# Kernel optimization log

Hardware: AMD Instinct MI355X
Metric: run time of the kernel (lower is better)

The kernel has to match this reference:

```python
import jax, jax.numpy as jnp
import numpy as np

EMBED_DIM = 768
NUM_HEAD = 12
HEAD_DIM = EMBED_DIM // NUM_HEAD


def setup_inputs() -> dict:
    key = jax.random.key(0)
    ks = jax.random.split(key, 9)
    B, S, E = 1, 4096, EMBED_DIM
    s = 1.0 / np.sqrt(E)
    inp = {
        "x": jax.random.normal(ks[0], (B, S, E), dtype=jnp.float32),
        "mask": jnp.zeros((B, S), dtype=jnp.bool_),  # True = masked out (padding)
        "Wq": jax.random.normal(ks[1], (E, E), dtype=jnp.float32) * s,
        "bq": jnp.zeros((E,), dtype=jnp.float32),
        "Wk": jax.random.normal(ks[2], (E, E), dtype=jnp.float32) * s,
        "bk": jnp.zeros((E,), dtype=jnp.float32),
        "Wv": jax.random.normal(ks[3], (E, E), dtype=jnp.float32) * s,
        "bv": jnp.zeros((E,), dtype=jnp.float32),
        "Wo": jax.random.normal(ks[4], (E, E), dtype=jnp.float32) * s,
        "bo": jnp.zeros((E,), dtype=jnp.float32),
    }
    return inp


def reference(x, mask, Wq, bq, Wk, bk, Wv, bv, Wo, bo):
    B, S, E = x.shape
    H, D = NUM_HEAD, HEAD_DIM
    # QKV projections -> [B, H, S, D]
    q = (x @ Wq.T + bq).reshape(B, S, H, D).transpose(0, 2, 1, 3)
    k = (x @ Wk.T + bk).reshape(B, S, H, D).transpose(0, 2, 1, 3)
    v = (x @ Wv.T + bv).reshape(B, S, H, D).transpose(0, 2, 1, 3)
    # NOTE: original scales by sqrt(embed_dim), not sqrt(head_dim)
    attn = jnp.einsum("bhqd,bhkd->bhqk", q, k) / jnp.sqrt(jnp.float32(E))
    # mask: [B, S] -> broadcast over (head, query) dims; True -> -inf
    attn = jnp.where(mask[:, None, None, :], -jnp.inf, attn)
    attn = jax.nn.softmax(attn, axis=-1)  # same math as manual max-subtract softmax
    out = jnp.einsum("bhqk,bhkd->bhqd", attn, v)  # [B, H, S, D]
    out = out.transpose(0, 2, 1, 3).reshape(B, S, E)
    return out @ Wo.T + bo
```

## Files before the change

kernel.cpp:

```cpp
#include <hip/hip_runtime.h>
#include <hip/hip_bf16.h>
#include <math.h>

typedef __bf16 bf16;
typedef __attribute__((ext_vector_type(8))) __bf16 bf16x8;
typedef __attribute__((ext_vector_type(4))) __bf16 bf16x4;
typedef __attribute__((ext_vector_type(4))) float f32x4;
typedef __attribute__((ext_vector_type(16))) float f32x16;

typedef __attribute__((address_space(1))) void* as1ptr;
typedef __attribute__((address_space(3))) void* as3ptr;

__device__ __forceinline__ void gload16(const void* g, void* lds) {
  __builtin_amdgcn_global_load_lds((as1ptr)(unsigned long long)(g),
                                   (as3ptr)(unsigned long long)(lds), 16, 0, 0);
}

#define MFMA16(a, b, c) __builtin_amdgcn_mfma_f32_16x16x32_bf16((a), (b), (c), 0, 0, 0)
#define MFMA32(a, b, c) __builtin_amdgcn_mfma_f32_32x32x16_bf16((a), (b), (c), 0, 0, 0)
#define EXP2(x) __builtin_amdgcn_exp2f(x)
#define WAITV4 asm volatile("s_waitcnt vmcnt(4)" ::: "memory")
#define WAITV2 asm volatile("s_waitcnt vmcnt(2)" ::: "memory")
#define WAITV0 asm volatile("s_waitcnt vmcnt(0)" ::: "memory")
#define BAR() __builtin_amdgcn_s_barrier()
#define PRIO1() __builtin_amdgcn_s_setprio(1)
#define PRIO0() __builtin_amdgcn_s_setprio(0)

#define SEQ 4096
#define EMB 768
#define QSC (0.036084391824351615f * 1.4426950408889634f)

#define NCVT 2688
__global__ __launch_bounds__(256)
void cvt_all_kernel(const float* __restrict__ x, const float* __restrict__ Wq,
                    const float* __restrict__ Wk, const float* __restrict__ Wv,
                    const float* __restrict__ Wo,
                    bf16* __restrict__ xb, bf16* __restrict__ Wqb, bf16* __restrict__ Wkb,
                    bf16* __restrict__ Wvb, bf16* __restrict__ Wob,
                    const unsigned char* __restrict__ mask,
                    unsigned long long* __restrict__ tf64) {
  int b = blockIdx.x;
  if (b == NCVT) {
    int t = threadIdx.x;
    if (t < 64) {
      unsigned v = 0;
      const unsigned char* mp = mask + t * 64;
      for (int i = 0; i < 64; i++) v |= mp[i];
      unsigned long long bits = __ballot(v != 0);
      if (t == 0) *tf64 = bits;
    }
    return;
  }
  const float* in;
  bf16* out;
  int base;
  if (b < 1536) {
    in = x; out = xb; base = b;
  } else {
    int r = b - 1536, seg = r / 288, off = r % 288;
    in  = (seg == 0) ? Wq  : (seg == 1) ? Wk  : (seg == 2) ? Wv  : Wo;
    out = (seg == 0) ? Wqb : (seg == 1) ? Wkb : (seg == 2) ? Wvb : Wob;
    base = off;
  }
  int i = (base * 256 + threadIdx.x) * 8;
  float4 a = *(const float4*)(in + i);
  float4 c = *(const float4*)(in + i + 4);
  bf16x8 v;
  v[0] = (bf16)a.x; v[1] = (bf16)a.y; v[2] = (bf16)a.z; v[3] = (bf16)a.w;
  v[4] = (bf16)c.x; v[5] = (bf16)c.y; v[6] = (bf16)c.z; v[7] = (bf16)c.w;
  *(bf16x8*)(out + i) = v;
}

template <int MODE>
__global__ __launch_bounds__(256)
void gemm_bt_kernel(const bf16* __restrict__ A,
                    const bf16* __restrict__ B0, const bf16* __restrict__ B1,
                    const bf16* __restrict__ B2,
                    const float* __restrict__ bias0, const float* __restrict__ bias1,
                    const float* __restrict__ bias2,
                    float* __restrict__ outF, bf16* __restrict__ Qh,
                    char* __restrict__ Kswz, char* __restrict__ Vswz) {
  __shared__ __attribute__((aligned(16))) char Asb[3][8192];
  __shared__ __attribute__((aligned(16))) char Bsb[3][8192];
  const int tid = threadIdx.x;
  const int wid = tid >> 6, lane = tid & 63;
  const int g = lane >> 4, c16 = lane & 15;
  const int wr = wid >> 1, wc = wid & 1;
  const int bm0 = blockIdx.x * 128;

  const bf16* Bp;
  const float* bias;
  int nb, mat = 0;
  if (MODE == 1) {
    mat = blockIdx.y / 6;
    nb = (blockIdx.y % 6) * 128;
    Bp = (mat == 0) ? B0 : (mat == 1 ? B1 : B2);
    bias = (mat == 0) ? bias0 : (mat == 1 ? bias1 : bias2);
  } else {
    nb = blockIdx.y * 128;
    Bp = B0;
    bias = bias0;
  }

  const int arow = tid >> 2, acol = (tid & 3) * 16;

#define STAGE_G(k, b)                                                              \
  do {                                                                             \
    gload16((const char*)A + (size_t)(bm0 + arow) * (EMB * 2) + (k)*64 + acol,     \
            &Asb[b][wid * 1024]);                                                  \
    gload16((const char*)A + (size_t)(bm0 + 64 + arow) * (EMB * 2) + (k)*64 + acol,\
            &Asb[b][4096 + wid * 1024]);                                           \
    gload16((const char*)Bp + (size_t)(nb + arow) * (EMB * 2) + (k)*64 + acol,     \
            &Bsb[b][wid * 1024]);                                                  \
    gload16((const char*)Bp + (size_t)(nb + 64 + arow) * (EMB * 2) + (k)*64 + acol,\
            &Bsb[b][4096 + wid * 1024]);                                           \
  } while (0)

  f32x4 acc[4][4];
#pragma unroll
  for (int i = 0; i < 4; i++)
#pragma unroll
    for (int j = 0; j < 4; j++) acc[i][j] = f32x4{0.f, 0.f, 0.f, 0.f};

#define COMPUTE_G(cur)                                                         \
  do {                                                                         \
    bf16x8 a[4], b[4];                                                         \
    _Pragma("unroll") for (int i = 0; i < 4; i++)                              \
        a[i] = *(const bf16x8*)(&Asb[cur][(wr * 64 + i * 16 + c16) * 64 + g * 16]); \
    _Pragma("unroll") for (int j = 0; j < 4; j++)                              \
        b[j] = *(const bf16x8*)(&Bsb[cur][(wc * 64 + j * 16 + c16) * 64 + g * 16]); \
    PRIO1();                                                                   \
    _Pragma("unroll") for (int i = 0; i < 4; i++)                              \
        _Pragma("unroll") for (int j = 0; j < 4; j++)                          \
            acc[i][j] = MFMA16(a[i], b[j], acc[i][j]);                         \
    PRIO0();                                                                   \
  } while (0)

  STAGE_G(0, 0);
  STAGE_G(1, 1);
  int cur = 0;
  for (int kk = 0; kk < EMB / 32 - 1; ++kk) {
    WAITV4;
    BAR();
    if (kk < EMB / 32 - 2) {
      int stb = (cur == 0) ? 2 : cur - 1;
      STAGE_G(kk + 2, stb);
    }
    COMPUTE_G(cur);
    cur = (cur == 2) ? 0 : cur + 1;
  }
  WAITV0;
  BAR();
  COMPUTE_G(cur);
#undef STAGE_G
#undef COMPUTE_G

#pragma unroll
  for (int i = 0; i < 4; i++) {
#pragma unroll
    for (int j = 0; j < 4; j++) {
      int colL = nb + wc * 64 + j * 16 + c16;
      float bval = bias[colL];
#pragma unroll
      for (int r = 0; r < 4; r++) {
        int row = bm0 + wr * 64 + i * 16 + 4 * g + r;
        float val = acc[i][j][r] + bval;
        if (MODE == 0) {
          outF[(size_t)row * EMB + colL] = val;
        } else {
          int hh = colL >> 6, d = colL & 63;
          if (mat == 0) {
            Qh[((size_t)hh * SEQ + row) * 64 + d] = (bf16)(val * QSC);
          } else if (mat == 1) {
            *(bf16*)(Kswz + ((size_t)hh * SEQ + row) * 128 +
                     ((d * 2) ^ ((row & 7) << 4))) = (bf16)val;
          } else {
            int kk2 = row & 63;
            int cc = (kk2 & 48) | (kk2 & 3) | ((kk2 & 4) << 1) | ((kk2 & 8) >> 1);
            *(bf16*)(Vswz + ((size_t)hh * 64 + d) * 8192 + (size_t)(row >> 6) * 128 +
                     ((cc * 2) ^ ((d & 7) << 4))) = (bf16)val;
          }
        }
      }
    }
  }
}

__global__ __launch_bounds__(512)
void attn_kernel(const char* __restrict__ Kswz, const char* __restrict__ Vswz,
                 const bf16* __restrict__ Qh, const unsigned char* __restrict__ mask,
                 const unsigned long long* __restrict__ tf64,
                 bf16* __restrict__ P0, bf16* __restrict__ P1, float* __restrict__ lm) {
  __shared__ __attribute__((aligned(16))) char LBUF[49152];
  char* LK = LBUF;
  char* LV = LBUF + 24576;
  const int tid = threadIdx.x;
  const int wid = tid >> 6, lane = tid & 63;
  const int qh = wid >> 1, kh = wid & 1;
  const int l31 = lane & 31, hi = lane >> 5;
  const int bsw = ((blockIdx.x & 7) * 96) + (blockIdx.x >> 3);
  const int h = bsw >> 6;
  const int rem = bsw & 63;
  const int qb = rem >> 1;
  const int ks = rem & 1;
  const unsigned long long tfb = *tf64;
  const int NT = 32;

  bf16x8 qa[4];
  {
    const bf16* qp = Qh + ((size_t)h * SEQ + qb * 128 + qh * 32 + l31) * 64 + hi * 8;
    qa[0] = *(const bf16x8*)(qp);
    qa[1] = *(const bf16x8*)(qp + 16);
    qa[2] = *(const bf16x8*)(qp + 32);
    qa[3] = *(const bf16x8*)(qp + 48);
  }

  f32x16 ot0, ot1;
#pragma unroll
  for (int r = 0; r < 16; r++) { ot0[r] = 0.f; ot1[r] = 0.f; }
  float m_ = -1e38f, l_ = 0.f;

  const char* ksrc = Kswz + (size_t)h * SEQ * 128 + (size_t)ks * 2048 * 128 + tid * 16;
  const char* vsrc = Vswz + ((size_t)h * 64 + (tid >> 3)) * 8192 + ks * 4096 + (tid & 7) * 16;

#define STAGE(t, b)                                              \
  do {                                                           \
    gload16(ksrc + (size_t)(t)*8192, LK + (b)*8192 + wid * 1024);\
    gload16(vsrc + (size_t)(t)*128,  LV + (b)*8192 + wid * 1024);\
  } while (0)

  const int krow = kh * 32 + l31;
  const int ksw = (krow & 7) << 4;
  const int vsw = (l31 & 7) << 4;
  const int vcb = kh * 64 + hi * 16;

#define COMPUTE(t, cur)                                                          \
  do {                                                                           \
    const char* Kb = LK + (cur)*8192;                                            \
    const char* Vb = LV + (cur)*8192;                                            \
    bf16x8 kf0 = *(const bf16x8*)(Kb + krow * 128 + ((hi * 16) ^ ksw));          \
    bf16x8 kf1 = *(const bf16x8*)(Kb + krow * 128 + ((32 + hi * 16) ^ ksw));     \
    bf16x8 kf2 = *(const bf16x8*)(Kb + krow * 128 + ((64 + hi * 16) ^ ksw));     \
    bf16x8 kf3 = *(const bf16x8*)(Kb + krow * 128 + ((96 + hi * 16) ^ ksw));     \
    f32x16 s;                                                                    \
    _Pragma("unroll") for (int r = 0; r < 16; r++) s[r] = 0.f;                   \
    PRIO1();                                                                     \
    s = MFMA32(kf0, qa[0], s);                                                   \
    s = MFMA32(kf1, qa[1], s);                                                   \
    s = MFMA32(kf2, qa[2], s);                                                   \
    s = MFMA32(kf3, qa[3], s);                                                   \
    PRIO0();                                                                     \
    if (tfb & (1ull << (ks * 32 + (t)))) {                                       \
      _Pragma("unroll") for (int r = 0; r < 16; r++) {                           \
        int key = ks * 2048 + (t)*64 + kh * 32 + (r & 3) + 8 * (r >> 2) + 4 * hi;\
        if (mask[key]) s[r] = -INFINITY;                                         \
      }                                                                          \
    }                                                                            \
    float m01 = fmaxf(fmaxf(s[0], s[1]), fmaxf(s[2], s[3]));                     \
    float m23 = fmaxf(fmaxf(s[4], s[5]), fmaxf(s[6], s[7]));                     \
    float m45 = fmaxf(fmaxf(s[8], s[9]), fmaxf(s[10], s[11]));                   \
    float m67 = fmaxf(fmaxf(s[12], s[13]), fmaxf(s[14], s[15]));                 \
    float mt = fmaxf(fmaxf(m01, m23), fmaxf(m45, m67));                          \
    mt = fmaxf(mt, __shfl_xor(mt, 32));                                          \
    if (__any(mt > m_ + 8.f)) {                                                  \
      float mn = fmaxf(m_, mt);                                                  \
      float corr = EXP2(m_ - mn);                                                \
      l_ *= corr;                                                                \
      ot0 *= corr;                                                               \
      ot1 *= corr;                                                               \
      m_ = mn;                                                                   \
    }                                                                            \
    float p[16];                                                                 \
    _Pragma("unroll") for (int r = 0; r < 16; r++) p[r] = EXP2(s[r] - m_);       \
    float ls = (((p[0] + p[1]) + (p[2] + p[3])) + ((p[4] + p[5]) + (p[6] + p[7]))) + \
               (((p[8] + p[9]) + (p[10] + p[11])) + ((p[12] + p[13]) + (p[14] + p[15]))); \
    ls += __shfl_xor(ls, 32);                                                    \
    l_ += ls;                                                                    \
    bf16x8 pb0, pb1;                                                             \
    _Pragma("unroll") for (int e = 0; e < 8; ++e) {                              \
      pb0[e] = (bf16)p[e];                                                       \
      pb1[e] = (bf16)p[8 + e];                                                   \
    }                                                                            \
    bf16x8 vf00 = *(const bf16x8*)(Vb + l31 * 128 + ((vcb) ^ vsw));              \
    bf16x8 vf01 = *(const bf16x8*)(Vb + l31 * 128 + ((vcb + 32) ^ vsw));         \
    bf16x8 vf10 = *(const bf16x8*)(Vb + (32 + l31) * 128 + ((vcb) ^ vsw));       \
    bf16x8 vf11 = *(const bf16x8*)(Vb + (32 + l31) * 128 + ((vcb + 32) ^ vsw));  \
    PRIO1();                                                                     \
    ot0 = MFMA32(vf00, pb0, ot0);                                                \
    ot0 = MFMA32(vf01, pb1, ot0);                                                \
    ot1 = MFMA32(vf10, pb0, ot1);                                                \
    ot1 = MFMA32(vf11, pb1, ot1);                                                \
    PRIO0();                                                                     \
  } while (0)

  STAGE(0, 0);
  STAGE(1, 1);
  int cur = 0;
  for (int t = 0; t < NT - 1; ++t) {
    WAITV2;
    BAR();
    if (t < NT - 2) {
      int stb = (cur == 0) ? 2 : cur - 1;
      STAGE(t + 2, stb);
    }
    COMPUTE(t, cur);
    cur = (cur == 2) ? 0 : cur + 1;
  }
  WAITV0;
  BAR();
  COMPUTE(NT - 1, cur);
#undef STAGE
#undef COMPUTE

  __syncthreads();
  float* ml = (float*)(LBUF + 32768);
  ml[(wid * 64 + lane) * 2 + 0] = m_;
  ml[(wid * 64 + lane) * 2 + 1] = l_;
  __syncthreads();
  const int pw = wid ^ 1;
  float m2 = ml[(pw * 64 + lane) * 2 + 0];
  float l2 = ml[(pw * 64 + lane) * 2 + 1];
  float M = fmaxf(m_, m2);
  float al = EXP2(m_ - M);
  float lt = al * l_ + EXP2(m2 - M) * l2;
  ot0 *= al;
  ot1 *= al;
  char* obase = LBUF + qh * 8192 + lane * 128;
  const int osw = (lane & 7) << 4;
  if (kh == 1) {
#pragma unroll
    for (int u = 0; u < 4; ++u) {
      f32x4 w0 = {ot0[4 * u], ot0[4 * u + 1], ot0[4 * u + 2], ot0[4 * u + 3]};
      f32x4 w1 = {ot1[4 * u], ot1[4 * u + 1], ot1[4 * u + 2], ot1[4 * u + 3]};
      *(f32x4*)(obase + ((u * 16) ^ osw)) = w0;
      *(f32x4*)(obase + (((4 + u) * 16) ^ osw)) = w1;
    }
  }
  __syncthreads();
  if (kh == 0) {
    float inv = 1.f / lt;
    int tok = qb * 128 + qh * 32 + l31;
    bf16* Op = ks ? P1 : P0;
    bf16* op = Op + (size_t)tok * EMB + h * 64;
#pragma unroll
    for (int u = 0; u < 4; ++u) {
      f32x4 w0 = *(const f32x4*)(obase + ((u * 16) ^ osw));
      f32x4 w1 = *(const f32x4*)(obase + (((4 + u) * 16) ^ osw));
      bf16x4 o0, o1;
#pragma unroll
      for (int e = 0; e < 4; ++e) {
        o0[e] = (bf16)((ot0[4 * u + e] + w0[e]) * inv);
        o1[e] = (bf16)((ot1[4 * u + e] + w1[e]) * inv);
      }
      *(bf16x4*)(op + 8 * u + 4 * hi) = o0;
      *(bf16x4*)(op + 32 + 8 * u + 4 * hi) = o1;
    }
    if (lane < 32) {
      float* lmp = lm + (((size_t)ks * 12 + h) * 4096 + tok) * 2;
      lmp[0] = M;
      lmp[1] = lt;
    }
  }
}

__global__ __launch_bounds__(256)
void merge_kernel(bf16* __restrict__ P0, const bf16* __restrict__ P1,
                  const float* __restrict__ lm) {
  int idx = (blockIdx.x * 256 + threadIdx.x) * 8;
  int tok = idx / EMB;
  int e0 = idx % EMB;
  int h = e0 >> 6;
  const float* l0p = lm + ((size_t)h * 4096 + tok) * 2;
  const float* l1p = lm + (((size_t)12 + h) * 4096 + tok) * 2;
  float m0 = l0p[0], l0 = l0p[1];
  float m1 = l1p[0], l1 = l1p[1];
  float M = fmaxf(m0, m1);
  float w0 = EXP2(m0 - M) * l0;
  float w1 = EXP2(m1 - M) * l1;
  float inv = 1.f / (w0 + w1);
  w0 *= inv;
  w1 *= inv;
  bf16x8 a = *(const bf16x8*)(P0 + idx);
  bf16x8 b = *(const bf16x8*)(P1 + idx);
  bf16x8 o;
#pragma unroll
  for (int e = 0; e < 8; ++e) o[e] = (bf16)(w0 * (float)a[e] + w1 * (float)b[e]);
  *(bf16x8*)(P0 + idx) = o;
}

extern "C" void kernel_launch(void* const* d_in, const int* in_sizes, int n_in,
                              void* d_out, int out_size, void* d_ws, size_t ws_size,
                              hipStream_t stream) {
  (void)in_sizes; (void)n_in; (void)out_size; (void)ws_size;
  const float* x = (const float*)d_in[0];
  const unsigned char* mask = (const unsigned char*)d_in[1];
  const float* Wq = (const float*)d_in[2];
  const float* bq = (const float*)d_in[3];
  const float* Wk = (const float*)d_in[4];
  const float* bk = (const float*)d_in[5];
  const float* Wv = (const float*)d_in[6];
  const float* bv = (const float*)d_in[7];
  const float* Wo = (const float*)d_in[8];
  const float* bo = (const float*)d_in[9];
  float* out = (float*)d_out;
  char* ws = (char*)d_ws;

  bf16* xb   = (bf16*)(ws + 0);
  bf16* Wqb  = (bf16*)(ws + 6291456);
  bf16* Wkb  = (bf16*)(ws + 7471104);
  bf16* Wvb  = (bf16*)(ws + 8650752);
  bf16* Wob  = (bf16*)(ws + 9830400);
  bf16* Qh   = (bf16*)(ws + 11010048);
  char* Kswz = ws + 17301504;
  char* Vswz = ws + 23592960;
  bf16* Obuf = (bf16*)(ws + 29884416);
  unsigned long long* tf64 = (unsigned long long*)(ws + 36175872);
  float* lmArr = (float*)(ws + 36179968);
  bf16* P1 = xb;

  cvt_all_kernel<<<NCVT + 1, 256, 0, stream>>>(x, Wq, Wk, Wv, Wo, xb, Wqb, Wkb, Wvb,
                                               Wob, mask, tf64);
  gemm_bt_kernel<1><<<dim3(32, 18), 256, 0, stream>>>(
      xb, Wqb, Wkb, Wvb, bq, bk, bv, nullptr, Qh, Kswz, Vswz);
  attn_kernel<<<768, 512, 0, stream>>>(Kswz, Vswz, Qh, mask, tf64, Obuf, P1, lmArr);
  merge_kernel<<<1536, 256, 0, stream>>>(Obuf, P1, lmArr);
  gemm_bt_kernel<0><<<dim3(32, 6), 256, 0, stream>>>(
      Obuf, Wob, nullptr, nullptr, bo, nullptr, nullptr, out, nullptr, nullptr, nullptr);
}
```

Measured before the change: 134.2 us.

## Process two query tiles per wave in attention and rotate K/V LDS layout

The attention kernel now runs 256 threads (4 waves) per block instead of 512. Each wave handles two 32-row query tiles, so every K and V fragment loaded from LDS feeds two MFMAs, and the staging loads per thread double. The K/V swizzle written by the projection GEMM gains a per-row block rotation, with matching read offsets, to spread LDS bank accesses. This raises register pressure from four output accumulators, and fewer waves per block may reduce latency hiding, which the launch bounds of 3 blocks per unit are meant to offset.

Measured after the change: 139.1 us. +3.7%, slower.

```diff
diff --git a/kernel.cpp b/kernel.cpp
--- a/kernel.cpp
+++ b/kernel.cpp
@@ -20,7 +20,6 @@
 #define MFMA32(a, b, c) __builtin_amdgcn_mfma_f32_32x32x16_bf16((a), (b), (c), 0, 0, 0)
 #define EXP2(x) __builtin_amdgcn_exp2f(x)
 #define WAITV4 asm volatile("s_waitcnt vmcnt(4)" ::: "memory")
-#define WAITV2 asm volatile("s_waitcnt vmcnt(2)" ::: "memory")
 #define WAITV0 asm volatile("s_waitcnt vmcnt(0)" ::: "memory")
 #define BAR() __builtin_amdgcn_s_barrier()
 #define PRIO1() __builtin_amdgcn_s_setprio(1)
@@ -172,13 +171,17 @@
           if (mat == 0) {
             Qh[((size_t)hh * SEQ + row) * 64 + d] = (bf16)(val * QSC);
           } else if (mat == 1) {
+            int blk = (((d * 2) >> 5) + (row >> 3)) & 3;
+            int off = blk * 32 + ((d * 2) & 31);
             *(bf16*)(Kswz + ((size_t)hh * SEQ + row) * 128 +
-                     ((d * 2) ^ ((row & 7) << 4))) = (bf16)val;
+                     (off ^ ((row & 7) << 4))) = (bf16)val;
           } else {
             int kk2 = row & 63;
             int cc = (kk2 & 48) | (kk2 & 3) | ((kk2 & 4) << 1) | ((kk2 & 8) >> 1);
+            int blk = (((cc * 2) >> 5) + (d >> 3)) & 3;
+            int off = blk * 32 + ((cc * 2) & 31);
             *(bf16*)(Vswz + ((size_t)hh * 64 + d) * 8192 + (size_t)(row >> 6) * 128 +
-                     ((cc * 2) ^ ((d & 7) << 4))) = (bf16)val;
+                     (off ^ ((d & 7) << 4))) = (bf16)val;
           }
         }
       }
@@ -186,7 +189,7 @@
   }
 }
 
-__global__ __launch_bounds__(512)
+__global__ __launch_bounds__(256, 3)
 void attn_kernel(const char* __restrict__ Kswz, const char* __restrict__ Vswz,
                  const bf16* __restrict__ Qh, const unsigned char* __restrict__ mask,
                  const unsigned long long* __restrict__ tf64,
@@ -206,90 +209,138 @@
   const unsigned long long tfb = *tf64;
   const int NT = 32;
 
-  bf16x8 qa[4];
+  bf16x8 qaA[4], qaB[4];
   {
-    const bf16* qp = Qh + ((size_t)h * SEQ + qb * 128 + qh * 32 + l31) * 64 + hi * 8;
-    qa[0] = *(const bf16x8*)(qp);
-    qa[1] = *(const bf16x8*)(qp + 16);
-    qa[2] = *(const bf16x8*)(qp + 32);
-    qa[3] = *(const bf16x8*)(qp + 48);
-  }
-
-  f32x16 ot0, ot1;
-#pragma unroll
-  for (int r = 0; r < 16; r++) { ot0[r] = 0.f; ot1[r] = 0.f; }
-  float m_ = -1e38f, l_ = 0.f;
+    const bf16* qp = Qh + ((size_t)h * SEQ + qb * 128 + qh * 64 + l31) * 64 + hi * 8;
+#pragma unroll
+    for (int j = 0; j < 4; ++j) {
+      qaA[j] = *(const bf16x8*)(qp + j * 16);
+      qaB[j] = *(const bf16x8*)(qp + 32 * 64 + j * 16);
+    }
+  }
+
+  f32x16 otA0, otA1, otB0, otB1;
+#pragma unroll
+  for (int r = 0; r < 16; r++) { otA0[r] = 0.f; otA1[r] = 0.f; otB0[r] = 0.f; otB1[r] = 0.f; }
+  float mA_ = -1e38f, lA_ = 0.f, mB_ = -1e38f, lB_ = 0.f;
 
   const char* ksrc = Kswz + (size_t)h * SEQ * 128 + (size_t)ks * 2048 * 128 + tid * 16;
   const char* vsrc = Vswz + ((size_t)h * 64 + (tid >> 3)) * 8192 + ks * 4096 + (tid & 7) * 16;
 
-#define STAGE(t, b)                                              \
-  do {                                                           \
-    gload16(ksrc + (size_t)(t)*8192, LK + (b)*8192 + wid * 1024);\
-    gload16(vsrc + (size_t)(t)*128,  LV + (b)*8192 + wid * 1024);\
+#define STAGE(t, b)                                                          \
+  do {                                                                       \
+    gload16(ksrc + (size_t)(t)*8192,        LK + (b)*8192 + wid * 1024);     \
+    gload16(ksrc + (size_t)(t)*8192 + 4096, LK + (b)*8192 + 4096 + wid * 1024); \
+    gload16(vsrc + (size_t)(t)*128,             LV + (b)*8192 + wid * 1024); \
+    gload16(vsrc + 32 * 8192 + (size_t)(t)*128, LV + (b)*8192 + 4096 + wid * 1024); \
   } while (0)
 
   const int krow = kh * 32 + l31;
   const int ksw = (krow & 7) << 4;
+  const int krot = (krow >> 3) & 3;
+  int kb_[4];
+#pragma unroll
+  for (int j = 0; j < 4; ++j) kb_[j] = ((((j + krot) & 3) * 32 + hi * 16) ^ ksw);
   const int vsw = (l31 & 7) << 4;
-  const int vcb = kh * 64 + hi * 16;
+  const int vrot = (l31 >> 3) & 3;
+  const int vb0 = (((kh * 2 + vrot) & 3) * 32 + hi * 16) ^ vsw;
+  const int vb1 = (((kh * 2 + 1 + vrot) & 3) * 32 + hi * 16) ^ vsw;
 
 #define COMPUTE(t, cur)                                                          \
   do {                                                                           \
     const char* Kb = LK + (cur)*8192;                                            \
     const char* Vb = LV + (cur)*8192;                                            \
-    bf16x8 kf0 = *(const bf16x8*)(Kb + krow * 128 + ((hi * 16) ^ ksw));          \
-    bf16x8 kf1 = *(const bf16x8*)(Kb + krow * 128 + ((32 + hi * 16) ^ ksw));     \
-    bf16x8 kf2 = *(const bf16x8*)(Kb + krow * 128 + ((64 + hi * 16) ^ ksw));     \
-    bf16x8 kf3 = *(const bf16x8*)(Kb + krow * 128 + ((96 + hi * 16) ^ ksw));     \
-    f32x16 s;                                                                    \
-    _Pragma("unroll") for (int r = 0; r < 16; r++) s[r] = 0.f;                   \
+    bf16x8 kf0 = *(const bf16x8*)(Kb + krow * 128 + kb_[0]);                     \
+    bf16x8 kf1 = *(const bf16x8*)(Kb + krow * 128 + kb_[1]);                     \
+    bf16x8 kf2 = *(const bf16x8*)(Kb + krow * 128 + kb_[2]);                     \
+    bf16x8 kf3 = *(const bf16x8*)(Kb + krow * 128 + kb_[3]);                     \
+    f32x16 sA, sB;                                                               \
+    _Pragma("unroll") for (int r = 0; r < 16; r++) { sA[r] = 0.f; sB[r] = 0.f; } \
     PRIO1();                                                                     \
-    s = MFMA32(kf0, qa[0], s);                                                   \
-    s = MFMA32(kf1, qa[1], s);                                                   \
-    s = MFMA32(kf2, qa[2], s);                                                   \
-    s = MFMA32(kf3, qa[3], s);                                                   \
+    sA = MFMA32(kf0, qaA[0], sA);                                                \
+    sB = MFMA32(kf0, qaB[0], sB);                                                \
+    sA = MFMA32(kf1, qaA[1], sA);                                                \
+    sB = MFMA32(kf1, qaB[1], sB);                                                \
+    sA = MFMA32(kf2, qaA[2], sA);                                                \
+    sB = MFMA32(kf2, qaB[2], sB);                                                \
+    sA = MFMA32(kf3, qaA[3], sA);                                                \
+    sB = MFMA32(kf3, qaB[3], sB);                                                \
     PRIO0();                                                                     \
     if (tfb & (1ull << (ks * 32 + (t)))) {                                       \
       _Pragma("unroll") for (int r = 0; r < 16; r++) {                           \
         int key = ks * 2048 + (t)*64 + kh * 32 + (r & 3) + 8 * (r >> 2) + 4 * hi;\
-        if (mask[key]) s[r] = -INFINITY;                                         \
+        if (mask[key]) { sA[r] = -INFINITY; sB[r] = -INFINITY; }                 \
       }                                                                          \
     }                                                                            \
-    float m01 = fmaxf(fmaxf(s[0], s[1]), fmaxf(s[2], s[3]));                     \
-    float m23 = fmaxf(fmaxf(s[4], s[5]), fmaxf(s[6], s[7]));                     \
-    float m45 = fmaxf(fmaxf(s[8], s[9]), fmaxf(s[10], s[11]));                   \
-    float m67 = fmaxf(fmaxf(s[12], s[13]), fmaxf(s[14], s[15]));                 \
-    float mt = fmaxf(fmaxf(m01, m23), fmaxf(m45, m67));                          \
-    mt = fmaxf(mt, __shfl_xor(mt, 32));                                          \
-    if (__any(mt > m_ + 8.f)) {                                                  \
-      float mn = fmaxf(m_, mt);                                                  \
-      float corr = EXP2(m_ - mn);                                                \
-      l_ *= corr;                                                                \
-      ot0 *= corr;                                                               \
-      ot1 *= corr;                                                               \
-      m_ = mn;                                                                   \
+    float mtA, mtB;                                                              \
+    {                                                                            \
+      float a0 = fmaxf(fmaxf(sA[0], sA[1]), fmaxf(sA[2], sA[3]));                \
+      float a1 = fmaxf(fmaxf(sA[4], sA[5]), fmaxf(sA[6], sA[7]));                \
+      float a2 = fmaxf(fmaxf(sA[8], sA[9]), fmaxf(sA[10], sA[11]));              \
+      float a3 = fmaxf(fmaxf(sA[12], sA[13]), fmaxf(sA[14], sA[15]));            \
+      mtA = fmaxf(fmaxf(a0, a1), fmaxf(a2, a3));                                 \
+      float b0 = fmaxf(fmaxf(sB[0], sB[1]), fmaxf(sB[2], sB[3]));                \
+      float b1 = fmaxf(fmaxf(sB[4], sB[5]), fmaxf(sB[6], sB[7]));                \
+      float b2 = fmaxf(fmaxf(sB[8], sB[9]), fmaxf(sB[10], sB[11]));              \
+      float b3 = fmaxf(fmaxf(sB[12], sB[13]), fmaxf(sB[14], sB[15]));            \
+      mtB = fmaxf(fmaxf(b0, b1), fmaxf(b2, b3));                                 \
     }                                                                            \
-    float p[16];                                                                 \
-    _Pragma("unroll") for (int r = 0; r < 16; r++) p[r] = EXP2(s[r] - m_);       \
-    float ls = (((p[0] + p[1]) + (p[2] + p[3])) + ((p[4] + p[5]) + (p[6] + p[7]))) + \
-               (((p[8] + p[9]) + (p[10] + p[11])) + ((p[12] + p[13]) + (p[14] + p[15]))); \
-    ls += __shfl_xor(ls, 32);                                                    \
-    l_ += ls;                                                                    \
-    bf16x8 pb0, pb1;                                                             \
-    _Pragma("unroll") for (int e = 0; e < 8; ++e) {                              \
-      pb0[e] = (bf16)p[e];                                                       \
-      pb1[e] = (bf16)p[8 + e];                                                   \
+    mtA = fmaxf(mtA, __shfl_xor(mtA, 32));                                       \
+    mtB = fmaxf(mtB, __shfl_xor(mtB, 32));                                       \
+    if (__any(mtA > mA_ + 8.f)) {                                                \
+      float mn = fmaxf(mA_, mtA);                                                \
+      float corr = EXP2(mA_ - mn);                                               \
+      lA_ *= corr;                                                               \
+      otA0 *= corr;                                                              \
+      otA1 *= corr;                                                              \
+      mA_ = mn;                                                                  \
     }                                                                            \
-    bf16x8 vf00 = *(const bf16x8*)(Vb + l31 * 128 + ((vcb) ^ vsw));              \
-    bf16x8 vf01 = *(const bf16x8*)(Vb + l31 * 128 + ((vcb + 32) ^ vsw));         \
-    bf16x8 vf10 = *(const bf16x8*)(Vb + (32 + l31) * 128 + ((vcb) ^ vsw));       \
-    bf16x8 vf11 = *(const bf16x8*)(Vb + (32 + l31) * 128 + ((vcb + 32) ^ vsw));  \
+    if (__any(mtB > mB_ + 8.f)) {                                                \
+      float mn = fmaxf(mB_, mtB);                                                \
+      float corr = EXP2(mB_ - mn);                                               \
+      lB_ *= corr;                                                               \
+      otB0 *= corr;                                                              \
+      otB1 *= corr;                                                              \
+      mB_ = mn;                                                                  \
+    }                                                                            \
+    bf16x8 pbA0, pbA1, pbB0, pbB1;                                               \
+    {                                                                            \
+      float p[16];                                                               \
+      _Pragma("unroll") for (int r = 0; r < 16; r++) p[r] = EXP2(sA[r] - mA_);   \
+      float ls = (((p[0] + p[1]) + (p[2] + p[3])) + ((p[4] + p[5]) + (p[6] + p[7]))) + \
+                 (((p[8] + p[9]) + (p[10] + p[11])) + ((p[12] + p[13]) + (p[14] + p[15]))); \
+      ls += __shfl_xor(ls, 32);                                                  \
+      lA_ += ls;                                                                 \
+      _Pragma("unroll") for (int e = 0; e < 8; ++e) {                            \
+        pbA0[e] = (bf16)p[e];                                                    \
+        pbA1[e] = (bf16)p[8 + e];                                                \
+      }                                                                          \
+    }                                                                            \
+    {                                                                            \
+      float p[16];                                                               \
+      _Pragma("unroll") for (int r = 0; r < 16; r++) p[r] = EXP2(sB[r] - mB_);   \
+      float ls = (((p[0] + p[1]) + (p[2] + p[3])) + ((p[4] + p[5]) + (p[6] + p[7]))) + \
+                 (((p[8] + p[9]) + (p[10] + p[11])) + ((p[12] + p[13]) + (p[14] + p[15]))); \
+      ls += __shfl_xor(ls, 32);                                                  \
+      lB_ += ls;                                                                 \
+      _Pragma("unroll") for (int e = 0; e < 8; ++e) {                            \
+        pbB0[e] = (bf16)p[e];                                                    \
+        pbB1[e] = (bf16)p[8 + e];                                                \
+      }                                                                          \
+    }                                                                            \
+    bf16x8 vf00 = *(const bf16x8*)(Vb + l31 * 128 + vb0);                        \
+    bf16x8 vf01 = *(const bf16x8*)(Vb + l31 * 128 + vb1);                        \
+    bf16x8 vf10 = *(const bf16x8*)(Vb + (32 + l31) * 128 + vb0);                 \
+    bf16x8 vf11 = *(const bf16x8*)(Vb + (32 + l31) * 128 + vb1);                 \
     PRIO1();                                                                     \
-    ot0 = MFMA32(vf00, pb0, ot0);                                                \
-    ot0 = MFMA32(vf01, pb1, ot0);                                                \
-    ot1 = MFMA32(vf10, pb0, ot1);                                                \
-    ot1 = MFMA32(vf11, pb1, ot1);                                                \
+    otA0 = MFMA32(vf00, pbA0, otA0);                                             \
+    otB0 = MFMA32(vf00, pbB0, otB0);                                             \
+    otA0 = MFMA32(vf01, pbA1, otA0);                                             \
+    otB0 = MFMA32(vf01, pbB1, otB0);                                             \
+    otA1 = MFMA32(vf10, pbA0, otA1);                                             \
+    otB1 = MFMA32(vf10, pbB0, otB1);                                             \
+    otA1 = MFMA32(vf11, pbA1, otA1);                                             \
+    otB1 = MFMA32(vf11, pbB1, otB1);                                             \
     PRIO0();                                                                     \
   } while (0)
 
@@ -297,7 +348,7 @@
   STAGE(1, 1);
   int cur = 0;
   for (int t = 0; t < NT - 1; ++t) {
-    WAITV2;
+    WAITV4;
     BAR();
     if (t < NT - 2) {
       int stb = (cur == 0) ? 2 : cur - 1;
@@ -314,51 +365,75 @@
 
   __syncthreads();
   float* ml = (float*)(LBUF + 32768);
-  ml[(wid * 64 + lane) * 2 + 0] = m_;
-  ml[(wid * 64 + lane) * 2 + 1] = l_;
+  {
+    float* p = ml + ((wid * 64 + lane) * 2) * 2;
+    p[0] = mA_; p[1] = lA_; p[2] = mB_; p[3] = lB_;
+  }
   __syncthreads();
   const int pw = wid ^ 1;
-  float m2 = ml[(pw * 64 + lane) * 2 + 0];
-  float l2 = ml[(pw * 64 + lane) * 2 + 1];
-  float M = fmaxf(m_, m2);
-  float al = EXP2(m_ - M);
-  float lt = al * l_ + EXP2(m2 - M) * l2;
-  ot0 *= al;
-  ot1 *= al;
-  char* obase = LBUF + qh * 8192 + lane * 128;
+  float ltA, ltB;
+  {
+    const float* p = ml + ((pw * 64 + lane) * 2) * 2;
+    float m2 = p[0], l2 = p[1];
+    float M = fmaxf(mA_, m2);
+    float al = EXP2(mA_ - M);
+    ltA = al * lA_ + EXP2(m2 - M) * l2;
+    otA0 *= al; otA1 *= al;
+    mA_ = M;
+    m2 = p[2]; l2 = p[3];
+    M = fmaxf(mB_, m2);
+    al = EXP2(mB_ - M);
+    ltB = al * lB_ + EXP2(m2 - M) * l2;
+    otB0 *= al; otB1 *= al;
+    mB_ = M;
+  }
+  char* baseA = LBUF + qh * 16384 + lane * 128;
+  char* baseB = LBUF + qh * 16384 + 8192 + lane * 128;
   const int osw = (lane & 7) << 4;
   if (kh == 1) {
 #pragma unroll
     for (int u = 0; u < 4; ++u) {
-      f32x4 w0 = {ot0[4 * u], ot0[4 * u + 1], ot0[4 * u + 2], ot0[4 * u + 3]};
-      f32x4 w1 = {ot1[4 * u], ot1[4 * u + 1], ot1[4 * u + 2], ot1[4 * u + 3]};
-      *(f32x4*)(obase + ((u * 16) ^ osw)) = w0;
-      *(f32x4*)(obase + (((4 + u) * 16) ^ osw)) = w1;
+      *(f32x4*)(baseA + ((u * 16) ^ osw)) =
+          f32x4{otA0[4 * u], otA0[4 * u + 1], otA0[4 * u + 2], otA0[4 * u + 3]};
+      *(f32x4*)(baseA + (((4 + u) * 16) ^ osw)) =
+          f32x4{otA1[4 * u], otA1[4 * u + 1], otA1[4 * u + 2], otA1[4 * u + 3]};
+      *(f32x4*)(baseB + ((u * 16) ^ osw)) =
+          f32x4{otB0[4 * u], otB0[4 * u + 1], otB0[4 * u + 2], otB0[4 * u + 3]};
+      *(f32x4*)(baseB + (((4 + u) * 16) ^ osw)) =
+          f32x4{otB1[4 * u], otB1[4 * u + 1], otB1[4 * u + 2], otB1[4 * u + 3]};
     }
   }
   __syncthreads();
   if (kh == 0) {
-    float inv = 1.f / lt;
-    int tok = qb * 128 + qh * 32 + l31;
     bf16* Op = ks ? P1 : P0;
-    bf16* op = Op + (size_t)tok * EMB + h * 64;
+    int tokA = qb * 128 + qh * 64 + l31;
+    float invA = 1.f / ltA, invB = 1.f / ltB;
+    bf16* opA = Op + (size_t)tokA * EMB + h * 64;
+    bf16* opB = Op + (size_t)(tokA + 32) * EMB + h * 64;
 #pragma unroll
     for (int u = 0; u < 4; ++u) {
-      f32x4 w0 = *(const f32x4*)(obase + ((u * 16) ^ osw));
-      f32x4 w1 = *(const f32x4*)(obase + (((4 + u) * 16) ^ osw));
-      bf16x4 o0, o1;
+      f32x4 wA0 = *(const f32x4*)(baseA + ((u * 16) ^ osw));
+      f32x4 wA1 = *(const f32x4*)(baseA + (((4 + u) * 16) ^ osw));
+      f32x4 wB0 = *(const f32x4*)(baseB + ((u * 16) ^ osw));
+      f32x4 wB1 = *(const f32x4*)(baseB + (((4 + u) * 16) ^ osw));
+      bf16x4 oA0, oA1, oB0, oB1;
 #pragma unroll
       for (int e = 0; e < 4; ++e) {
-        o0[e] = (bf16)((ot0[4 * u + e] + w0[e]) * inv);
-        o1[e] = (bf16)((ot1[4 * u + e] + w1[e]) * inv);
+        oA0[e] = (bf16)((otA0[4 * u + e] + wA0[e]) * invA);
+        oA1[e] = (bf16)((otA1[4 * u + e] + wA1[e]) * invA);
+        oB0[e] = (bf16)((otB0[4 * u + e] + wB0[e]) * invB);
+        oB1[e] = (bf16)((otB1[4 * u + e] + wB1[e]) * invB);
       }
-      *(bf16x4*)(op + 8 * u + 4 * hi) = o0;
-      *(bf16x4*)(op + 32 + 8 * u + 4 * hi) = o1;
+      *(bf16x4*)(opA + 8 * u + 4 * hi) = oA0;
+      *(bf16x4*)(opA + 32 + 8 * u + 4 * hi) = oA1;
+      *(bf16x4*)(opB + 8 * u + 4 * hi) = oB0;
+      *(bf16x4*)(opB + 32 + 8 * u + 4 * hi) = oB1;
     }
     if (lane < 32) {
-      float* lmp = lm + (((size_t)ks * 12 + h) * 4096 + tok) * 2;
-      lmp[0] = M;
-      lmp[1] = lt;
+      float* lmpA = lm + (((size_t)ks * 12 + h) * 4096 + tokA) * 2;
+      lmpA[0] = mA_; lmpA[1] = ltA;
+      float* lmpB = lm + (((size_t)ks * 12 + h) * 4096 + tokA + 32) * 2;
+      lmpB[0] = mB_; lmpB[1] = ltB;
     }
   }
 }
@@ -422,7 +497,7 @@
                                                Wob, mask, tf64);
   gemm_bt_kernel<1><<<dim3(32, 18), 256, 0, stream>>>(
       xb, Wqb, Wkb, Wvb, bq, bk, bv, nullptr, Qh, Kswz, Vswz);
-  attn_kernel<<<768, 512, 0, stream>>>(Kswz, Vswz, Qh, mask, tf64, Obuf, P1, lmArr);
+  attn_kernel<<<768, 256, 0, stream>>>(Kswz, Vswz, Qh, mask, tf64, Obuf, P1, lmArr);
   merge_kernel<<<1536, 256, 0, stream>>>(Obuf, P1, lmArr);
   gemm_bt_kernel<0><<<dim3(32, 6), 256, 0, stream>>>(
       Obuf, Wob, nullptr, nullptr, bo, nullptr, nullptr, out, nullptr, nullptr, nullptr);
```

## Software-pipeline QK^T of next tile with softmax and PV of previous tile

Applied to the files above, without the earlier changes.

Splits the attention inner loop into a QK^T part and a softmax+PV part. The QK^T MFMAs for tile t now run alongside the softmax and PV for tile t-1, so matrix work can overlap the exp and reduction VALU work. The K/V staging schedule changes to match, with an extra barrier per iteration so the buffer just consumed can be safely overwritten. This keeps two score accumulators live, raising register pressure, and the added barrier may cost some synchronization time.

Result: slower. 151.3 us (+12.8%).

```diff
diff --git a/kernel.cpp b/kernel.cpp
--- a/kernel.cpp
+++ b/kernel.cpp
@@ -234,32 +234,41 @@
   const int vsw = (l31 & 7) << 4;
   const int vcb = kh * 64 + hi * 16;
 
-#define COMPUTE(t, cur)                                                          \
+  f32x16 sP, sC;
+
+#define QKPART(t, cur, sDST)                                                     \
   do {                                                                           \
     const char* Kb = LK + (cur)*8192;                                            \
-    const char* Vb = LV + (cur)*8192;                                            \
     bf16x8 kf0 = *(const bf16x8*)(Kb + krow * 128 + ((hi * 16) ^ ksw));          \
     bf16x8 kf1 = *(const bf16x8*)(Kb + krow * 128 + ((32 + hi * 16) ^ ksw));     \
     bf16x8 kf2 = *(const bf16x8*)(Kb + krow * 128 + ((64 + hi * 16) ^ ksw));     \
     bf16x8 kf3 = *(const bf16x8*)(Kb + krow * 128 + ((96 + hi * 16) ^ ksw));     \
-    f32x16 s;                                                                    \
-    _Pragma("unroll") for (int r = 0; r < 16; r++) s[r] = 0.f;                   \
+    _Pragma("unroll") for (int r = 0; r < 16; r++) sDST[r] = 0.f;                \
     PRIO1();                                                                     \
-    s = MFMA32(kf0, qa[0], s);                                                   \
-    s = MFMA32(kf1, qa[1], s);                                                   \
-    s = MFMA32(kf2, qa[2], s);                                                   \
-    s = MFMA32(kf3, qa[3], s);                                                   \
+    sDST = MFMA32(kf0, qa[0], sDST);                                             \
+    sDST = MFMA32(kf1, qa[1], sDST);                                             \
+    sDST = MFMA32(kf2, qa[2], sDST);                                             \
+    sDST = MFMA32(kf3, qa[3], sDST);                                             \
     PRIO0();                                                                     \
     if (tfb & (1ull << (ks * 32 + (t)))) {                                       \
       _Pragma("unroll") for (int r = 0; r < 16; r++) {                           \
         int key = ks * 2048 + (t)*64 + kh * 32 + (r & 3) + 8 * (r >> 2) + 4 * hi;\
-        if (mask[key]) s[r] = -INFINITY;                                         \
+        if (mask[key]) sDST[r] = -INFINITY;                                      \
       }                                                                          \
     }                                                                            \
-    float m01 = fmaxf(fmaxf(s[0], s[1]), fmaxf(s[2], s[3]));                     \
-    float m23 = fmaxf(fmaxf(s[4], s[5]), fmaxf(s[6], s[7]));                     \
-    float m45 = fmaxf(fmaxf(s[8], s[9]), fmaxf(s[10], s[11]));                   \
-    float m67 = fmaxf(fmaxf(s[12], s[13]), fmaxf(s[14], s[15]));                 \
+  } while (0)
+
+#define SOFTPV(curV)                                                             \
+  do {                                                                           \
+    const char* Vb = LV + (curV)*8192;                                           \
+    bf16x8 vf00 = *(const bf16x8*)(Vb + l31 * 128 + ((vcb) ^ vsw));              \
+    bf16x8 vf01 = *(const bf16x8*)(Vb + l31 * 128 + ((vcb + 32) ^ vsw));         \
+    bf16x8 vf10 = *(const bf16x8*)(Vb + (32 + l31) * 128 + ((vcb) ^ vsw));       \
+    bf16x8 vf11 = *(const bf16x8*)(Vb + (32 + l31) * 128 + ((vcb + 32) ^ vsw));  \
+    float m01 = fmaxf(fmaxf(sP[0], sP[1]), fmaxf(sP[2], sP[3]));                 \
+    float m23 = fmaxf(fmaxf(sP[4], sP[5]), fmaxf(sP[6], sP[7]));                 \
+    float m45 = fmaxf(fmaxf(sP[8], sP[9]), fmaxf(sP[10], sP[11]));               \
+    float m67 = fmaxf(fmaxf(sP[12], sP[13]), fmaxf(sP[14], sP[15]));             \
     float mt = fmaxf(fmaxf(m01, m23), fmaxf(m45, m67));                          \
     mt = fmaxf(mt, __shfl_xor(mt, 32));                                          \
     if (__any(mt > m_ + 8.f)) {                                                  \
@@ -270,21 +279,16 @@
       ot1 *= corr;                                                               \
       m_ = mn;                                                                   \
     }                                                                            \
-    float p[16];                                                                 \
-    _Pragma("unroll") for (int r = 0; r < 16; r++) p[r] = EXP2(s[r] - m_);       \
-    float ls = (((p[0] + p[1]) + (p[2] + p[3])) + ((p[4] + p[5]) + (p[6] + p[7]))) + \
-               (((p[8] + p[9]) + (p[10] + p[11])) + ((p[12] + p[13]) + (p[14] + p[15]))); \
+    _Pragma("unroll") for (int r = 0; r < 16; r++) sP[r] = EXP2(sP[r] - m_);     \
+    float ls = (((sP[0] + sP[1]) + (sP[2] + sP[3])) + ((sP[4] + sP[5]) + (sP[6] + sP[7]))) + \
+               (((sP[8] + sP[9]) + (sP[10] + sP[11])) + ((sP[12] + sP[13]) + (sP[14] + sP[15]))); \
     ls += __shfl_xor(ls, 32);                                                    \
     l_ += ls;                                                                    \
     bf16x8 pb0, pb1;                                                             \
     _Pragma("unroll") for (int e = 0; e < 8; ++e) {                              \
-      pb0[e] = (bf16)p[e];                                                       \
-      pb1[e] = (bf16)p[8 + e];                                                   \
+      pb0[e] = (bf16)sP[e];                                                      \
+      pb1[e] = (bf16)sP[8 + e];                                                  \
     }                                                                            \
-    bf16x8 vf00 = *(const bf16x8*)(Vb + l31 * 128 + ((vcb) ^ vsw));              \
-    bf16x8 vf01 = *(const bf16x8*)(Vb + l31 * 128 + ((vcb + 32) ^ vsw));         \
-    bf16x8 vf10 = *(const bf16x8*)(Vb + (32 + l31) * 128 + ((vcb) ^ vsw));       \
-    bf16x8 vf11 = *(const bf16x8*)(Vb + (32 + l31) * 128 + ((vcb + 32) ^ vsw));  \
     PRIO1();                                                                     \
     ot0 = MFMA32(vf00, pb0, ot0);                                                \
     ot0 = MFMA32(vf01, pb1, ot0);                                                \
@@ -295,22 +299,26 @@
 
   STAGE(0, 0);
   STAGE(1, 1);
-  int cur = 0;
-  for (int t = 0; t < NT - 1; ++t) {
-    WAITV2;
+  WAITV2;
+  BAR();
+  STAGE(2, 2);
+  QKPART(0, 0, sP);
+  int curT = 1, prev = 0;
+  for (int t = 1; t < NT; ++t) {
+    if (t < NT - 1) { WAITV2; } else { WAITV0; }
     BAR();
-    if (t < NT - 2) {
-      int stb = (cur == 0) ? 2 : cur - 1;
-      STAGE(t + 2, stb);
-    }
-    COMPUTE(t, cur);
-    cur = (cur == 2) ? 0 : cur + 1;
-  }
-  WAITV0;
-  BAR();
-  COMPUTE(NT - 1, cur);
+    QKPART(t, curT, sC);
+    SOFTPV(prev);
+    sP = sC;
+    BAR();
+    if (t <= NT - 3) STAGE(t + 2, prev);
+    prev = curT;
+    curT = (curT == 2) ? 0 : curT + 1;
+  }
+  SOFTPV(prev);
 #undef STAGE
-#undef COMPUTE
+#undef QKPART
+#undef SOFTPV
 
   __syncthreads();
   float* ml = (float*)(LBUF + 32768);
@@ -330,10 +338,10 @@
   if (kh == 1) {
 #pragma unroll
     for (int u = 0; u < 4; ++u) {
-      f32x4 w0 = {ot0[4 * u], ot0[4 * u + 1], ot0[4 * u + 2], ot0[4 * u + 3]};
-      f32x4 w1 = {ot1[4 * u], ot1[4 * u + 1], ot1[4 * u + 2], ot1[4 * u + 3]};
-      *(f32x4*)(obase + ((u * 16) ^ osw)) = w0;
-      *(f32x4*)(obase + (((4 + u) * 16) ^ osw)) = w1;
+      *(f32x4*)(obase + ((u * 16) ^ osw)) =
+          f32x4{ot0[4 * u], ot0[4 * u + 1], ot0[4 * u + 2], ot0[4 * u + 3]};
+      *(f32x4*)(obase + (((4 + u) * 16) ^ osw)) =
+          f32x4{ot1[4 * u], ot1[4 * u + 1], ot1[4 * u + 2], ot1[4 * u + 3]};
     }
   }
   __syncthreads();
```
